# Kernel optimization log

Hardware: AMD Instinct MI355X
Metric: run time of the kernel (lower is better)

## Reference

```python
import jax, jax.numpy as jnp
import numpy as np

N_NODES = 100000
N_EDGES = 1600000
NFEAT, NHID, NCLASS = 512, 256, 128
K_HOPS = 5
ALPHA = 0.1


def setup_inputs() -> dict:
    key = jax.random.key(0)
    ks = jax.random.split(key, 7)
    x = jax.random.normal(ks[0], (N_NODES, NFEAT), dtype=jnp.float32)
    edge_index = jax.random.randint(ks[1], (2, N_EDGES), 0, N_NODES, dtype=jnp.int64)
    edge_weight = jax.random.uniform(ks[2], (N_EDGES,), dtype=jnp.float32)
    # Glorot-ish scaled linear weights
    W1 = jax.random.normal(ks[3], (NFEAT, NHID), dtype=jnp.float32) * (1.0 / np.sqrt(NFEAT))
    b1 = jnp.zeros((NHID,), dtype=jnp.float32)
    W2 = jax.random.normal(ks[4], (NHID, NCLASS), dtype=jnp.float32) * (1.0 / np.sqrt(NHID))
    b2 = jnp.zeros((NCLASS,), dtype=jnp.float32)
    return {"x": x, "edge_index": edge_index, "edge_weight": edge_weight,
            "W1": W1, "b1": b1, "W2": W2, "b2": b2}


def reference(x, edge_index, edge_weight, W1, b1, W2, b2):
    # 2-layer MLP (act after first layer only; dropout p=0)
    h = jnp.maximum(x @ W1 + b1, 0.0)
    h = h @ W2 + b2  # [N, nclass]
    src = edge_index[0]
    dst = edge_index[1]
    x0 = h

    def step(carry, _):
        # gather by source, scale by edge weight, scatter-add at target
        msg = carry[src] * edge_weight[:, None]          # [E, nclass]
        agg = jax.ops.segment_sum(msg, dst, num_segments=N_NODES)
        out = (1.0 - ALPHA) * agg + ALPHA * x0           # restart mix
        return out, None

    xK, _ = jax.lax.scan(step, x0, None, length=K_HOPS)
    return jax.nn.log_softmax(xK, axis=1)
```

## Files before the change

kernel.cpp:

```cpp
#include <hip/hip_runtime.h>
#include <hip/hip_bf16.h>
#include <cstdint>
#include <cstddef>

#define N_NODES 100000
#define NFEAT 512
#define NHID 256
#define NCLASS 128
#define K_HOPS 5
#define ALPHA 0.1f

typedef __attribute__((ext_vector_type(8))) short short8v;
typedef __attribute__((ext_vector_type(4))) float f32x4;

__device__ __forceinline__ unsigned short f2bf(float f) {
    unsigned u = __builtin_bit_cast(unsigned, f);
    u += 0x7FFFu + ((u >> 16) & 1u);
    return (unsigned short)(u >> 16);
}
__device__ __forceinline__ float bflo(unsigned u) {
    return __builtin_bit_cast(float, u << 16);
}
__device__ __forceinline__ float bfhi(unsigned u) {
    return __builtin_bit_cast(float, u & 0xFFFF0000u);
}
__device__ __forceinline__ unsigned cvtpk2(float a, float b) {
    unsigned r;
    asm("v_cvt_pk_bf16_f32 %0, %1, %2" : "=v"(r) : "v"(a), "v"(b));
    return r;
}
__device__ __forceinline__ void gload_lds16(const void* g, void* l) {
    __builtin_amdgcn_global_load_lds((const __attribute__((address_space(1))) void*)g,
                                     (__attribute__((address_space(3))) void*)l, 16, 0, 0);
}


__global__ void count_kernel(const int* __restrict__ dst, int* __restrict__ counts, int E) {
    int i = blockIdx.x * blockDim.x + threadIdx.x;
    if (i < E) atomicAdd(&counts[dst[i]], 1);
}

__global__ __launch_bounds__(256) void scan_p1(const int* __restrict__ counts,
                                               int* __restrict__ partial, int n) {
    __shared__ int ws[4];
    int b = blockIdx.x, t = threadIdx.x;
    int base = b * 1024 + t * 4;
    int s = 0;
#pragma unroll
    for (int j = 0; j < 4; ++j) {
        int idx = base + j;
        if (idx < n) s += counts[idx];
    }
#pragma unroll
    for (int off = 32; off; off >>= 1) s += __shfl_xor(s, off, 64);
    if ((t & 63) == 0) ws[t >> 6] = s;
    __syncthreads();
    if (t == 0) partial[b] = ws[0] + ws[1] + ws[2] + ws[3];
}

__global__ __launch_bounds__(128) void scan_p2(int* __restrict__ partial, int nb) {
    __shared__ int s[128];
    int t = threadIdx.x;
    int v = (t < nb) ? partial[t] : 0;
    s[t] = v;
    __syncthreads();
    for (int off = 1; off < 128; off <<= 1) {
        int u = (t >= off) ? s[t - off] : 0;
        __syncthreads();
        s[t] += u;
        __syncthreads();
    }
    if (t < nb) partial[t] = (t == 0) ? 0 : s[t - 1];
}

__global__ __launch_bounds__(256) void scan_p3(const int* __restrict__ counts,
                                               const int* __restrict__ partial,
                                               int* __restrict__ row_ptr,
                                               int* __restrict__ fill, int n) {
    __shared__ int ts[256];
    int b = blockIdx.x, t = threadIdx.x;
    int base = b * 1024 + t * 4;
    int c[4];
#pragma unroll
    for (int j = 0; j < 4; ++j) {
        int idx = base + j;
        c[j] = (idx < n) ? counts[idx] : 0;
    }
    int s = c[0] + c[1] + c[2] + c[3];
    ts[t] = s;
    __syncthreads();
    for (int off = 1; off < 256; off <<= 1) {
        int v = (t >= off) ? ts[t - off] : 0;
        __syncthreads();
        ts[t] += v;
        __syncthreads();
    }
    int pre = partial[b] + ((t == 0) ? 0 : ts[t - 1]);
#pragma unroll
    for (int j = 0; j < 4; ++j) {
        int idx = base + j;
        if (idx < n) {
            row_ptr[idx] = pre;
            fill[idx] = pre;
            if (idx == n - 1) row_ptr[n] = pre + c[j];
            pre += c[j];
        }
    }
}

__global__ void scatter_kernel(const int* __restrict__ src, const int* __restrict__ dst,
                               const float* __restrict__ w, int* __restrict__ fill,
                               int2* __restrict__ epk, int E) {
    int i = blockIdx.x * blockDim.x + threadIdx.x;
    if (i < E) {
        int d = dst[i];
        int pos = atomicAdd(&fill[d], 1);
        int2 m; m.x = src[i]; m.y = __builtin_bit_cast(int, w[i]);
        epk[pos] = m;
    }
}

__global__ void wtrans_kernel(const float* __restrict__ W, unsigned short* __restrict__ Wt,
                              int K, int N) {
    int idx = blockIdx.x * blockDim.x + threadIdx.x;
    if (idx >= N * K) return;
    int n = idx / K, k = idx - n * K;
    Wt[idx] = f2bf(W[(size_t)k * N + n]);
}

__global__ __launch_bounds__(512) void gemm1_pipe(const float* __restrict__ X,
                                                  const unsigned short* __restrict__ W1t,
                                                  const float* __restrict__ b1,
                                                  unsigned short* __restrict__ Hb, int M) {
    __shared__ char smem[131072];
    char* const Ab0 = smem;
    char* const Bb0 = smem + 65536;

    const int tid = threadIdx.x;
    const int lane = tid & 63;
    const int wv = tid >> 6;
    const int wr = wv >> 2, wc = wv & 3;
    const int brow = blockIdx.x * 128;

    const char* asrc[2];
    int adst[2];
#pragma unroll
    for (int c = 0; c < 2; ++c) {
        int ar = brow + wv * 16 + (lane & 15); if (ar > M - 1) ar = M - 1;
        int k = (lane >> 4) * 8 + c * 4;
        asrc[c] = (const char*)&X[(size_t)ar * NFEAT + k];
        adst[c] = (wv + c * 8) * 1024;
    }
    const char* bsrc[2];
    int bdst[2];
#pragma unroll
    for (int c = 0; c < 2; ++c) {
        int ci = wv + c * 8;
        int col = ci * 16 + (lane & 15);
        bsrc[c] = (const char*)&W1t[(size_t)col * NFEAT + (lane >> 4) * 8];
        bdst[c] = ci * 1024;
    }

    f32x4 acc[4][4];
#pragma unroll
    for (int m = 0; m < 4; ++m)
#pragma unroll
        for (int n = 0; n < 4; ++n) acc[m][n] = f32x4{0.f, 0.f, 0.f, 0.f};

    auto stage = [&](int buf, int step) {
#pragma unroll
        for (int c = 0; c < 2; ++c)
            gload_lds16(asrc[c] + (size_t)step * 128, Ab0 + buf * 16384 + adst[c]);
#pragma unroll
        for (int c = 0; c < 2; ++c)
            gload_lds16(bsrc[c] + (size_t)step * 64, Bb0 + buf * 16384 + bdst[c]);
    };

    constexpr int NSTEP = NFEAT / 32;
    stage(0, 0);
    stage(1, 1);

    for (int s = 0; s < NSTEP; ++s) {
        if (s + 2 < NSTEP) {
            stage((s + 2) & 3, s + 2);
            asm volatile("s_waitcnt vmcnt(8)" ::: "memory");
        } else if (s + 1 < NSTEP) {
            asm volatile("s_waitcnt vmcnt(4)" ::: "memory");
        } else {
            asm volatile("s_waitcnt vmcnt(0)" ::: "memory");
        }
        __builtin_amdgcn_s_barrier();
        asm volatile("" ::: "memory");

        const char* Abuf = Ab0 + (s & 3) * 16384;
        const char* Bbuf = Bb0 + (s & 3) * 16384;
        short8v a[4], b[4];
#pragma unroll
        for (int m = 0; m < 4; ++m) {
            int g = ((wr * 4 + m) * 64 + lane) * 16;
            f32x4 lo = *(const f32x4*)(Abuf + g);
            f32x4 hi = *(const f32x4*)(Abuf + 8192 + g);
            uint4 u;
            u.x = cvtpk2(lo[0], lo[1]); u.y = cvtpk2(lo[2], lo[3]);
            u.z = cvtpk2(hi[0], hi[1]); u.w = cvtpk2(hi[2], hi[3]);
            a[m] = __builtin_bit_cast(short8v, u);
        }
#pragma unroll
        for (int n = 0; n < 4; ++n)
            b[n] = *(const short8v*)(Bbuf + ((wc * 4 + n) * 64 + lane) * 16);
#pragma unroll
        for (int m = 0; m < 4; ++m)
#pragma unroll
            for (int n = 0; n < 4; ++n)
                acc[m][n] = __builtin_amdgcn_mfma_f32_16x16x32_bf16(a[m], b[n], acc[m][n], 0, 0, 0);

        __builtin_amdgcn_s_barrier();
        asm volatile("" ::: "memory");
    }

#pragma unroll
    for (int n = 0; n < 4; ++n) {
        int colg = wc * 64 + n * 16 + (lane & 15);
        float bv = b1[colg];
#pragma unroll
        for (int m = 0; m < 4; ++m) {
#pragma unroll
            for (int r = 0; r < 4; ++r) {
                int rowg = brow + wr * 64 + m * 16 + (lane >> 4) * 4 + r;
                if (rowg < M) {
                    float v = fmaxf(acc[m][n][r] + bv, 0.f);
                    Hb[(size_t)rowg * NHID + colg] = f2bf(v);
                }
            }
        }
    }
}

__global__ __launch_bounds__(256) void gemm2_pipe(const unsigned short* __restrict__ Hb,
                                                  const unsigned short* __restrict__ W2t,
                                                  const float* __restrict__ b2,
                                                  unsigned short* __restrict__ C0, int M) {
    __shared__ char smem[65536];
    char* const Ab0 = smem;
    char* const Bb0 = smem + 32768;

    const int tid = threadIdx.x;
    const int lane = tid & 63;
    const int wv = tid >> 6;
    const int wr = wv >> 1, wc = wv & 1;
    const int brow = blockIdx.x * 128;

    const char* asrc[2];
    const char* bsrc[2];
    int adst[2], bdst[2];
#pragma unroll
    for (int c = 0; c < 2; ++c) {
        int ci = wv + c * 4;
        int ar = brow + ci * 16 + (lane & 15); if (ar > M - 1) ar = M - 1;
        asrc[c] = (const char*)&Hb[(size_t)ar * NHID + (lane >> 4) * 8];
        adst[c] = ci * 1024;
        int col = ci * 16 + (lane & 15);
        bsrc[c] = (const char*)&W2t[(size_t)col * NHID + (lane >> 4) * 8];
        bdst[c] = ci * 1024;
    }

    f32x4 acc[4][4];
#pragma unroll
    for (int m = 0; m < 4; ++m)
#pragma unroll
        for (int n = 0; n < 4; ++n) acc[m][n] = f32x4{0.f, 0.f, 0.f, 0.f};

    auto stage = [&](int buf, int step) {
#pragma unroll
        for (int c = 0; c < 2; ++c)
            gload_lds16(asrc[c] + (size_t)step * 64, Ab0 + buf * 8192 + adst[c]);
#pragma unroll
        for (int c = 0; c < 2; ++c)
            gload_lds16(bsrc[c] + (size_t)step * 64, Bb0 + buf * 8192 + bdst[c]);
    };

    constexpr int NSTEP = NHID / 32;
    stage(0, 0);
    stage(1, 1);

    for (int s = 0; s < NSTEP; ++s) {
        if (s + 2 < NSTEP) {
            stage((s + 2) & 3, s + 2);
            asm volatile("s_waitcnt vmcnt(8)" ::: "memory");
        } else if (s + 1 < NSTEP) {
            asm volatile("s_waitcnt vmcnt(4)" ::: "memory");
        } else {
            asm volatile("s_waitcnt vmcnt(0)" ::: "memory");
        }
        __builtin_amdgcn_s_barrier();
        asm volatile("" ::: "memory");

        const char* Abuf = Ab0 + (s & 3) * 8192;
        const char* Bbuf = Bb0 + (s & 3) * 8192;
        short8v a[4], b[4];
#pragma unroll
        for (int m = 0; m < 4; ++m)
            a[m] = *(const short8v*)(Abuf + ((wr * 4 + m) * 64 + lane) * 16);
#pragma unroll
        for (int n = 0; n < 4; ++n)
            b[n] = *(const short8v*)(Bbuf + ((wc * 4 + n) * 64 + lane) * 16);
#pragma unroll
        for (int m = 0; m < 4; ++m)
#pragma unroll
            for (int n = 0; n < 4; ++n)
                acc[m][n] = __builtin_amdgcn_mfma_f32_16x16x32_bf16(a[m], b[n], acc[m][n], 0, 0, 0);

        __builtin_amdgcn_s_barrier();
        asm volatile("" ::: "memory");
    }

#pragma unroll
    for (int n = 0; n < 4; ++n) {
        int colg = wc * 64 + n * 16 + (lane & 15);
        float bv = b2[colg];
#pragma unroll
        for (int m = 0; m < 4; ++m) {
#pragma unroll
            for (int r = 0; r < 4; ++r) {
                int rowg = brow + wr * 64 + m * 16 + (lane >> 4) * 4 + r;
                if (rowg < M)
                    C0[(size_t)rowg * NCLASS + colg] = f2bf(acc[m][n][r] + bv);
            }
        }
    }
}

template<int FINAL>
__global__ __launch_bounds__(256) void hop_kernel(const unsigned short* __restrict__ carry,
                                                  const unsigned short* __restrict__ c0,
                                                  const int* __restrict__ rp,
                                                  const int2* __restrict__ epk,
                                                  unsigned short* __restrict__ outb,
                                                  float* __restrict__ outf, int nnodes) {
    int node = blockIdx.x * 4 + (threadIdx.x >> 6);
    if (node >= nnodes) return;
    int lane = threadIdx.x & 63;
    int e0 = rp[node], e1 = rp[node + 1];

    float a0x = 0.f, a0y = 0.f, a1x = 0.f, a1y = 0.f;
    float a2x = 0.f, a2y = 0.f, a3x = 0.f, a3y = 0.f;

    for (int eb = e0; eb < e1; eb += 64) {
        int nb = e1 - eb; if (nb > 64) nb = 64;
        int cs = 0, wvi = 0;
        if (lane < nb) {
            int2 m = epk[eb + lane];
            cs = m.x; wvi = m.y;
        }
        int j = 0;
        for (; j + 7 < nb; j += 8) {
            int s0 = __builtin_amdgcn_readlane(cs, j);
            int s1 = __builtin_amdgcn_readlane(cs, j + 1);
            int s2 = __builtin_amdgcn_readlane(cs, j + 2);
            int s3 = __builtin_amdgcn_readlane(cs, j + 3);
            int s4 = __builtin_amdgcn_readlane(cs, j + 4);
            int s5 = __builtin_amdgcn_readlane(cs, j + 5);
            int s6 = __builtin_amdgcn_readlane(cs, j + 6);
            int s7 = __builtin_amdgcn_readlane(cs, j + 7);
            float w0 = __builtin_bit_cast(float, __builtin_amdgcn_readlane(wvi, j));
            float w1 = __builtin_bit_cast(float, __builtin_amdgcn_readlane(wvi, j + 1));
            float w2 = __builtin_bit_cast(float, __builtin_amdgcn_readlane(wvi, j + 2));
            float w3 = __builtin_bit_cast(float, __builtin_amdgcn_readlane(wvi, j + 3));
            float w4 = __builtin_bit_cast(float, __builtin_amdgcn_readlane(wvi, j + 4));
            float w5 = __builtin_bit_cast(float, __builtin_amdgcn_readlane(wvi, j + 5));
            float w6 = __builtin_bit_cast(float, __builtin_amdgcn_readlane(wvi, j + 6));
            float w7 = __builtin_bit_cast(float, __builtin_amdgcn_readlane(wvi, j + 7));
            unsigned u0 = ((const unsigned*)(carry + ((size_t)s0 << 7)))[lane];
            unsigned u1 = ((const unsigned*)(carry + ((size_t)s1 << 7)))[lane];
            unsigned u2 = ((const unsigned*)(carry + ((size_t)s2 << 7)))[lane];
            unsigned u3 = ((const unsigned*)(carry + ((size_t)s3 << 7)))[lane];
            unsigned u4 = ((const unsigned*)(carry + ((size_t)s4 << 7)))[lane];
            unsigned u5 = ((const unsigned*)(carry + ((size_t)s5 << 7)))[lane];
            unsigned u6 = ((const unsigned*)(carry + ((size_t)s6 << 7)))[lane];
            unsigned u7 = ((const unsigned*)(carry + ((size_t)s7 << 7)))[lane];
            a0x = fmaf(w0, bflo(u0), a0x); a0y = fmaf(w0, bfhi(u0), a0y);
            a1x = fmaf(w1, bflo(u1), a1x); a1y = fmaf(w1, bfhi(u1), a1y);
            a2x = fmaf(w2, bflo(u2), a2x); a2y = fmaf(w2, bfhi(u2), a2y);
            a3x = fmaf(w3, bflo(u3), a3x); a3y = fmaf(w3, bfhi(u3), a3y);
            a0x = fmaf(w4, bflo(u4), a0x); a0y = fmaf(w4, bfhi(u4), a0y);
            a1x = fmaf(w5, bflo(u5), a1x); a1y = fmaf(w5, bfhi(u5), a1y);
            a2x = fmaf(w6, bflo(u6), a2x); a2y = fmaf(w6, bfhi(u6), a2y);
            a3x = fmaf(w7, bflo(u7), a3x); a3y = fmaf(w7, bfhi(u7), a3y);
        }
        for (; j + 3 < nb; j += 4) {
            int s0 = __builtin_amdgcn_readlane(cs, j);
            int s1 = __builtin_amdgcn_readlane(cs, j + 1);
            int s2 = __builtin_amdgcn_readlane(cs, j + 2);
            int s3 = __builtin_amdgcn_readlane(cs, j + 3);
            float w0 = __builtin_bit_cast(float, __builtin_amdgcn_readlane(wvi, j));
            float w1 = __builtin_bit_cast(float, __builtin_amdgcn_readlane(wvi, j + 1));
            float w2 = __builtin_bit_cast(float, __builtin_amdgcn_readlane(wvi, j + 2));
            float w3 = __builtin_bit_cast(float, __builtin_amdgcn_readlane(wvi, j + 3));
            unsigned u0 = ((const unsigned*)(carry + ((size_t)s0 << 7)))[lane];
            unsigned u1 = ((const unsigned*)(carry + ((size_t)s1 << 7)))[lane];
            unsigned u2 = ((const unsigned*)(carry + ((size_t)s2 << 7)))[lane];
            unsigned u3 = ((const unsigned*)(carry + ((size_t)s3 << 7)))[lane];
            a0x = fmaf(w0, bflo(u0), a0x); a0y = fmaf(w0, bfhi(u0), a0y);
            a1x = fmaf(w1, bflo(u1), a1x); a1y = fmaf(w1, bfhi(u1), a1y);
            a2x = fmaf(w2, bflo(u2), a2x); a2y = fmaf(w2, bfhi(u2), a2y);
            a3x = fmaf(w3, bflo(u3), a3x); a3y = fmaf(w3, bfhi(u3), a3y);
        }
        for (; j < nb; ++j) {
            int s0 = __builtin_amdgcn_readlane(cs, j);
            float w0 = __builtin_bit_cast(float, __builtin_amdgcn_readlane(wvi, j));
            unsigned u0 = ((const unsigned*)(carry + ((size_t)s0 << 7)))[lane];
            a0x = fmaf(w0, bflo(u0), a0x); a0y = fmaf(w0, bfhi(u0), a0y);
        }
    }

    unsigned ux = ((const unsigned*)(c0 + ((size_t)node << 7)))[lane];
    float vx = (1.f - ALPHA) * (a0x + a1x + a2x + a3x) + ALPHA * bflo(ux);
    float vy = (1.f - ALPHA) * (a0y + a1y + a2y + a3y) + ALPHA * bfhi(ux);

    if (FINAL) {
        float mx = fmaxf(vx, vy);
#pragma unroll
        for (int off = 32; off; off >>= 1) mx = fmaxf(mx, __shfl_xor(mx, off, 64));
        float se = __expf(vx - mx) + __expf(vy - mx);
#pragma unroll
        for (int off = 32; off; off >>= 1) se += __shfl_xor(se, off, 64);
        float l = mx + __logf(se);
        float2 o; o.x = vx - l; o.y = vy - l;
        ((float2*)(outf + ((size_t)node << 7)))[lane] = o;
    } else {
        unsigned o = (unsigned)f2bf(vx) | ((unsigned)f2bf(vy) << 16);
        ((unsigned*)(outb + ((size_t)node << 7)))[lane] = o;
    }
}


extern "C" void kernel_launch(void* const* d_in, const int* in_sizes, int n_in,
                              void* d_out, int out_size, void* d_ws, size_t ws_size,
                              hipStream_t stream) {
    const float* x   = (const float*)d_in[0];
    const int*   ei  = (const int*)d_in[1];
    const float* ew  = (const float*)d_in[2];
    const float* W1  = (const float*)d_in[3];
    const float* b1  = (const float*)d_in[4];
    const float* W2  = (const float*)d_in[5];
    const float* b2  = (const float*)d_in[6];
    float* outp = (float*)d_out;

    const int E = in_sizes[1] / 2;
    const int Nn = N_NODES;
    const int* srcv = ei;
    const int* dstv = ei + E;
    const size_t NC = (size_t)Nn * NCLASS;

    unsigned short* c0  = (unsigned short*)d_ws;
    unsigned short* A16 = c0 + NC;
    unsigned short* B16 = A16 + NC;
    unsigned short* hb  = A16;
    unsigned short* w1t = B16 + NC;
    unsigned short* w2t = w1t + NHID * NFEAT;
    int* row_ptr = (int*)(w2t + NCLASS * NHID);
    int* fill    = row_ptr + (Nn + 1);
    int* partial = fill + Nn;
    int2* epk    = (int2*)(partial + 128);

    const int NB = (Nn + 1023) / 1024;

    hipMemsetAsync(fill, 0, (size_t)Nn * sizeof(int), stream);
    count_kernel<<<(E + 255) / 256, 256, 0, stream>>>(dstv, fill, E);
    scan_p1<<<NB, 256, 0, stream>>>(fill, partial, Nn);
    scan_p2<<<1, 128, 0, stream>>>(partial, NB);
    scan_p3<<<NB, 256, 0, stream>>>(fill, partial, row_ptr, fill, Nn);
    scatter_kernel<<<(E + 255) / 256, 256, 0, stream>>>(srcv, dstv, ew, fill, epk, E);

    wtrans_kernel<<<(NHID * NFEAT + 255) / 256, 256, 0, stream>>>(W1, w1t, NFEAT, NHID);
    wtrans_kernel<<<(NCLASS * NHID + 255) / 256, 256, 0, stream>>>(W2, w2t, NHID, NCLASS);

    {
        int gm = (Nn + 127) / 128;
        gemm1_pipe<<<gm, 512, 0, stream>>>(x, w1t, b1, hb, Nn);
        gemm2_pipe<<<gm, 256, 0, stream>>>(hb, w2t, b2, c0, Nn);
    }

    int grid = (Nn + 3) / 4;
    const unsigned short* carry = c0;
    unsigned short* dsts[2] = {A16, B16};
    for (int k = 0; k < K_HOPS - 1; ++k) {
        unsigned short* o = dsts[k & 1];
        hop_kernel<0><<<grid, 256, 0, stream>>>(carry, c0, row_ptr, epk, o, nullptr, Nn);
        carry = o;
    }
    hop_kernel<1><<<grid, 256, 0, stream>>>(carry, c0, row_ptr, epk, nullptr, outp, Nn);
}
```

Baseline: 640.4 us.

## Split hop gather into 4 column groups with edge-parallel subwaves

The SpMM hop kernel is restructured so each wave handles one 64-byte column slice (32 features) of a node, with a grid dimension over 4 column groups. The 4 sub-groups of 16 lanes each process different edges in parallel and reduce with cross-lane shuffles. The aim is more memory-level parallelism and more waves for short-degree nodes. The cost is that each node's edge list and row pointers are read 4 times, and 3/4 of the lanes sit idle on the epilogue. Log-softmax moves to a separate kernel, which adds an extra pass over the output.

After: 0.9996 ms. +56.1%, slower.

```diff
diff --git a/kernel.cpp b/kernel.cpp
--- a/kernel.cpp
+++ b/kernel.cpp
@@ -331,106 +331,80 @@
 }
 
 template<int FINAL>
-__global__ __launch_bounds__(256) void hop_kernel(const unsigned short* __restrict__ carry,
-                                                  const unsigned short* __restrict__ c0,
-                                                  const int* __restrict__ rp,
-                                                  const int2* __restrict__ epk,
-                                                  unsigned short* __restrict__ outb,
-                                                  float* __restrict__ outf, int nnodes) {
+__global__ __launch_bounds__(256) void hop_grp(const unsigned short* __restrict__ carry,
+                                               const unsigned short* __restrict__ c0,
+                                               const int* __restrict__ rp,
+                                               const int2* __restrict__ epk,
+                                               unsigned short* __restrict__ outb,
+                                               float* __restrict__ outf, int nnodes) {
+    int node = blockIdx.x * 4 + (threadIdx.x >> 6);
+    if (node >= nnodes) return;
+    const int g = blockIdx.y;
+    const int lane = threadIdx.x & 63;
+    const int sub = lane >> 4;
+    const int c = lane & 15;
+    const int gbase = g * 16 + c;
+    const unsigned* cu = (const unsigned*)carry;
+
+    int e0 = rp[node], e1 = rp[node + 1];
+    float ax = 0.f, ay = 0.f;
+
+    for (int eb = e0; eb < e1; eb += 64) {
+        int nb = e1 - eb; if (nb > 64) nb = 64;
+        int cs = 0, wv = 0;
+        if (lane < nb) {
+            int2 m = epk[eb + lane];
+            cs = m.x; wv = m.y;
+        }
+        for (int j = 0; j < nb; j += 16) {
+            int i0 = j + sub, i1 = i0 + 4, i2 = i0 + 8, i3 = i0 + 12;
+            int s0 = __shfl(cs, i0, 64); float w0 = __builtin_bit_cast(float, __shfl(wv, i0, 64));
+            int s1 = __shfl(cs, i1, 64); float w1 = __builtin_bit_cast(float, __shfl(wv, i1, 64));
+            int s2 = __shfl(cs, i2, 64); float w2 = __builtin_bit_cast(float, __shfl(wv, i2, 64));
+            int s3 = __shfl(cs, i3, 64); float w3 = __builtin_bit_cast(float, __shfl(wv, i3, 64));
+            unsigned u0 = cu[(size_t)s0 * 64 + gbase];
+            unsigned u1 = cu[(size_t)s1 * 64 + gbase];
+            unsigned u2 = cu[(size_t)s2 * 64 + gbase];
+            unsigned u3 = cu[(size_t)s3 * 64 + gbase];
+            ax = fmaf(w0, bflo(u0), ax); ay = fmaf(w0, bfhi(u0), ay);
+            ax = fmaf(w1, bflo(u1), ax); ay = fmaf(w1, bfhi(u1), ay);
+            ax = fmaf(w2, bflo(u2), ax); ay = fmaf(w2, bfhi(u2), ay);
+            ax = fmaf(w3, bflo(u3), ax); ay = fmaf(w3, bfhi(u3), ay);
+        }
+    }
+
+    ax += __shfl_xor(ax, 16, 64); ax += __shfl_xor(ax, 32, 64);
+    ay += __shfl_xor(ay, 16, 64); ay += __shfl_xor(ay, 32, 64);
+
+    if (lane < 16) {
+        unsigned u = ((const unsigned*)c0)[(size_t)node * 64 + gbase];
+        float vx = (1.f - ALPHA) * ax + ALPHA * bflo(u);
+        float vy = (1.f - ALPHA) * ay + ALPHA * bfhi(u);
+        if (FINAL) {
+            float2 o; o.x = vx; o.y = vy;
+            ((float2*)outf)[(size_t)node * 64 + gbase] = o;
+        } else {
+            ((unsigned*)outb)[(size_t)node * 64 + gbase] =
+                (unsigned)f2bf(vx) | ((unsigned)f2bf(vy) << 16);
+        }
+    }
+}
+
+__global__ __launch_bounds__(256) void logsoftmax_kernel(float* __restrict__ buf, int nnodes) {
     int node = blockIdx.x * 4 + (threadIdx.x >> 6);
     if (node >= nnodes) return;
     int lane = threadIdx.x & 63;
-    int e0 = rp[node], e1 = rp[node + 1];
-
-    float a0x = 0.f, a0y = 0.f, a1x = 0.f, a1y = 0.f;
-    float a2x = 0.f, a2y = 0.f, a3x = 0.f, a3y = 0.f;
-
-    for (int eb = e0; eb < e1; eb += 64) {
-        int nb = e1 - eb; if (nb > 64) nb = 64;
-        int cs = 0, wvi = 0;
-        if (lane < nb) {
-            int2 m = epk[eb + lane];
-            cs = m.x; wvi = m.y;
-        }
-        int j = 0;
-        for (; j + 7 < nb; j += 8) {
-            int s0 = __builtin_amdgcn_readlane(cs, j);
-            int s1 = __builtin_amdgcn_readlane(cs, j + 1);
-            int s2 = __builtin_amdgcn_readlane(cs, j + 2);
-            int s3 = __builtin_amdgcn_readlane(cs, j + 3);
-            int s4 = __builtin_amdgcn_readlane(cs, j + 4);
-            int s5 = __builtin_amdgcn_readlane(cs, j + 5);
-            int s6 = __builtin_amdgcn_readlane(cs, j + 6);
-            int s7 = __builtin_amdgcn_readlane(cs, j + 7);
-            float w0 = __builtin_bit_cast(float, __builtin_amdgcn_readlane(wvi, j));
-            float w1 = __builtin_bit_cast(float, __builtin_amdgcn_readlane(wvi, j + 1));
-            float w2 = __builtin_bit_cast(float, __builtin_amdgcn_readlane(wvi, j + 2));
-            float w3 = __builtin_bit_cast(float, __builtin_amdgcn_readlane(wvi, j + 3));
-            float w4 = __builtin_bit_cast(float, __builtin_amdgcn_readlane(wvi, j + 4));
-            float w5 = __builtin_bit_cast(float, __builtin_amdgcn_readlane(wvi, j + 5));
-            float w6 = __builtin_bit_cast(float, __builtin_amdgcn_readlane(wvi, j + 6));
-            float w7 = __builtin_bit_cast(float, __builtin_amdgcn_readlane(wvi, j + 7));
-            unsigned u0 = ((const unsigned*)(carry + ((size_t)s0 << 7)))[lane];
-            unsigned u1 = ((const unsigned*)(carry + ((size_t)s1 << 7)))[lane];
-            unsigned u2 = ((const unsigned*)(carry + ((size_t)s2 << 7)))[lane];
-            unsigned u3 = ((const unsigned*)(carry + ((size_t)s3 << 7)))[lane];
-            unsigned u4 = ((const unsigned*)(carry + ((size_t)s4 << 7)))[lane];
-            unsigned u5 = ((const unsigned*)(carry + ((size_t)s5 << 7)))[lane];
-            unsigned u6 = ((const unsigned*)(carry + ((size_t)s6 << 7)))[lane];
-            unsigned u7 = ((const unsigned*)(carry + ((size_t)s7 << 7)))[lane];
-            a0x = fmaf(w0, bflo(u0), a0x); a0y = fmaf(w0, bfhi(u0), a0y);
-            a1x = fmaf(w1, bflo(u1), a1x); a1y = fmaf(w1, bfhi(u1), a1y);
-            a2x = fmaf(w2, bflo(u2), a2x); a2y = fmaf(w2, bfhi(u2), a2y);
-            a3x = fmaf(w3, bflo(u3), a3x); a3y = fmaf(w3, bfhi(u3), a3y);
-            a0x = fmaf(w4, bflo(u4), a0x); a0y = fmaf(w4, bfhi(u4), a0y);
-            a1x = fmaf(w5, bflo(u5), a1x); a1y = fmaf(w5, bfhi(u5), a1y);
-            a2x = fmaf(w6, bflo(u6), a2x); a2y = fmaf(w6, bfhi(u6), a2y);
-            a3x = fmaf(w7, bflo(u7), a3x); a3y = fmaf(w7, bfhi(u7), a3y);
-        }
-        for (; j + 3 < nb; j += 4) {
-            int s0 = __builtin_amdgcn_readlane(cs, j);
-            int s1 = __builtin_amdgcn_readlane(cs, j + 1);
-            int s2 = __builtin_amdgcn_readlane(cs, j + 2);
-            int s3 = __builtin_amdgcn_readlane(cs, j + 3);
-            float w0 = __builtin_bit_cast(float, __builtin_amdgcn_readlane(wvi, j));
-            float w1 = __builtin_bit_cast(float, __builtin_amdgcn_readlane(wvi, j + 1));
-            float w2 = __builtin_bit_cast(float, __builtin_amdgcn_readlane(wvi, j + 2));
-            float w3 = __builtin_bit_cast(float, __builtin_amdgcn_readlane(wvi, j + 3));
-            unsigned u0 = ((const unsigned*)(carry + ((size_t)s0 << 7)))[lane];
-            unsigned u1 = ((const unsigned*)(carry + ((size_t)s1 << 7)))[lane];
-            unsigned u2 = ((const unsigned*)(carry + ((size_t)s2 << 7)))[lane];
-            unsigned u3 = ((const unsigned*)(carry + ((size_t)s3 << 7)))[lane];
-            a0x = fmaf(w0, bflo(u0), a0x); a0y = fmaf(w0, bfhi(u0), a0y);
-            a1x = fmaf(w1, bflo(u1), a1x); a1y = fmaf(w1, bfhi(u1), a1y);
-            a2x = fmaf(w2, bflo(u2), a2x); a2y = fmaf(w2, bfhi(u2), a2y);
-            a3x = fmaf(w3, bflo(u3), a3x); a3y = fmaf(w3, bfhi(u3), a3y);
-        }
-        for (; j < nb; ++j) {
-            int s0 = __builtin_amdgcn_readlane(cs, j);
-            float w0 = __builtin_bit_cast(float, __builtin_amdgcn_readlane(wvi, j));
-            unsigned u0 = ((const unsigned*)(carry + ((size_t)s0 << 7)))[lane];
-            a0x = fmaf(w0, bflo(u0), a0x); a0y = fmaf(w0, bfhi(u0), a0y);
-        }
-    }
-
-    unsigned ux = ((const unsigned*)(c0 + ((size_t)node << 7)))[lane];
-    float vx = (1.f - ALPHA) * (a0x + a1x + a2x + a3x) + ALPHA * bflo(ux);
-    float vy = (1.f - ALPHA) * (a0y + a1y + a2y + a3y) + ALPHA * bfhi(ux);
-
-    if (FINAL) {
-        float mx = fmaxf(vx, vy);
-#pragma unroll
-        for (int off = 32; off; off >>= 1) mx = fmaxf(mx, __shfl_xor(mx, off, 64));
-        float se = __expf(vx - mx) + __expf(vy - mx);
-#pragma unroll
-        for (int off = 32; off; off >>= 1) se += __shfl_xor(se, off, 64);
-        float l = mx + __logf(se);
-        float2 o; o.x = vx - l; o.y = vy - l;
-        ((float2*)(outf + ((size_t)node << 7)))[lane] = o;
-    } else {
-        unsigned o = (unsigned)f2bf(vx) | ((unsigned)f2bf(vy) << 16);
-        ((unsigned*)(outb + ((size_t)node << 7)))[lane] = o;
-    }
+    float2* p = (float2*)(buf + ((size_t)node << 7)) + lane;
+    float2 v = *p;
+    float m = fmaxf(v.x, v.y);
+#pragma unroll
+    for (int off = 32; off; off >>= 1) m = fmaxf(m, __shfl_xor(m, off, 64));
+    float s = __expf(v.x - m) + __expf(v.y - m);
+#pragma unroll
+    for (int off = 32; off; off >>= 1) s += __shfl_xor(s, off, 64);
+    float l = m + __logf(s);
+    float2 o; o.x = v.x - l; o.y = v.y - l;
+    *p = o;
 }
 
 
@@ -481,13 +455,15 @@
         gemm2_pipe<<<gm, 256, 0, stream>>>(hb, w2t, b2, c0, Nn);
     }
 
-    int grid = (Nn + 3) / 4;
+    dim3 gh((Nn + 3) / 4, 4);
     const unsigned short* carry = c0;
     unsigned short* dsts[2] = {A16, B16};
     for (int k = 0; k < K_HOPS - 1; ++k) {
         unsigned short* o = dsts[k & 1];
-        hop_kernel<0><<<grid, 256, 0, stream>>>(carry, c0, row_ptr, epk, o, nullptr, Nn);
+        hop_grp<0><<<gh, 256, 0, stream>>>(carry, c0, row_ptr, epk, o, nullptr, Nn);
         carry = o;
     }
-    hop_kernel<1><<<grid, 256, 0, stream>>>(carry, c0, row_ptr, epk, nullptr, outp, Nn);
-}
+    hop_grp<1><<<gh, 256, 0, stream>>>(carry, c0, row_ptr, epk, nullptr, outp, Nn);
+
+    logsoftmax_kernel<<<(Nn + 3) / 4, 256, 0, stream>>>(outp, Nn);
+}
```

## Replace multi-buffered GEMM pipelines with single-buffer, smaller-tile GEMM kernels

Applied to the files above, without the earlier changes.

Both MLP GEMM kernels drop the 4-stage async LDS pipeline in favour of a simple load, wait, sync, compute loop with a single LDS buffer. GEMM1 also splits the 256 output columns over two blocks, using 256-thread blocks with 128x128 tiles instead of 512-thread blocks covering all 256 columns. This cuts LDS use per block (128KB to 24KB, 64KB to 16KB) so more blocks can be resident, relying on occupancy rather than software prefetch to hide latency. The cost is exposed load latency inside each block and GEMM1 reading the fp32 X tiles twice.

New measurement: 691.0 us. 1.08x slower.

```diff
diff --git a/kernel.cpp b/kernel.cpp
--- a/kernel.cpp
+++ b/kernel.cpp
@@ -128,35 +128,37 @@
     Wt[idx] = f2bf(W[(size_t)k * N + n]);
 }
 
-__global__ __launch_bounds__(512) void gemm1_pipe(const float* __restrict__ X,
-                                                  const unsigned short* __restrict__ W1t,
-                                                  const float* __restrict__ b1,
-                                                  unsigned short* __restrict__ Hb, int M) {
-    __shared__ char smem[131072];
-    char* const Ab0 = smem;
-    char* const Bb0 = smem + 65536;
+__global__ __launch_bounds__(256) void gemm1_m97(const float* __restrict__ X,
+                                                 const unsigned short* __restrict__ W1t,
+                                                 const float* __restrict__ b1,
+                                                 unsigned short* __restrict__ Hb, int M) {
+    __shared__ char smem[24576];
+    char* const Abuf = smem;
+    char* const Bbuf = smem + 16384;
 
     const int tid = threadIdx.x;
     const int lane = tid & 63;
     const int wv = tid >> 6;
-    const int wr = wv >> 2, wc = wv & 3;
-    const int brow = blockIdx.x * 128;
-
-    const char* asrc[2];
-    int adst[2];
-#pragma unroll
-    for (int c = 0; c < 2; ++c) {
-        int ar = brow + wv * 16 + (lane & 15); if (ar > M - 1) ar = M - 1;
-        int k = (lane >> 4) * 8 + c * 4;
-        asrc[c] = (const char*)&X[(size_t)ar * NFEAT + k];
-        adst[c] = (wv + c * 8) * 1024;
+    const int wr = wv >> 1, wc = wv & 1;
+    const int bcol = blockIdx.x * 128;
+    const int brow = blockIdx.y * 128;
+
+    const char* asrc[4];
+    int adst[4];
+#pragma unroll
+    for (int c = 0; c < 4; ++c) {
+        int ci = wv + c * 4;
+        int sub = ci & 7, plane = ci >> 3;
+        int ar = brow + sub * 16 + (lane & 15); if (ar > M - 1) ar = M - 1;
+        asrc[c] = (const char*)&X[(size_t)ar * NFEAT + (lane >> 4) * 8 + plane * 4];
+        adst[c] = ci * 1024;
     }
     const char* bsrc[2];
     int bdst[2];
 #pragma unroll
     for (int c = 0; c < 2; ++c) {
-        int ci = wv + c * 8;
-        int col = ci * 16 + (lane & 15);
+        int ci = wv + c * 4;
+        int col = bcol + ci * 16 + (lane & 15);
         bsrc[c] = (const char*)&W1t[(size_t)col * NFEAT + (lane >> 4) * 8];
         bdst[c] = ci * 1024;
     }
@@ -167,33 +169,16 @@
 #pragma unroll
         for (int n = 0; n < 4; ++n) acc[m][n] = f32x4{0.f, 0.f, 0.f, 0.f};
 
-    auto stage = [&](int buf, int step) {
+    for (int s = 0; s < NFEAT / 32; ++s) {
+#pragma unroll
+        for (int c = 0; c < 4; ++c)
+            gload_lds16(asrc[c] + (size_t)s * 128, Abuf + adst[c]);
 #pragma unroll
         for (int c = 0; c < 2; ++c)
-            gload_lds16(asrc[c] + (size_t)step * 128, Ab0 + buf * 16384 + adst[c]);
-#pragma unroll
-        for (int c = 0; c < 2; ++c)
-            gload_lds16(bsrc[c] + (size_t)step * 64, Bb0 + buf * 16384 + bdst[c]);
-    };
-
-    constexpr int NSTEP = NFEAT / 32;
-    stage(0, 0);
-    stage(1, 1);
-
-    for (int s = 0; s < NSTEP; ++s) {
-        if (s + 2 < NSTEP) {
-            stage((s + 2) & 3, s + 2);
-            asm volatile("s_waitcnt vmcnt(8)" ::: "memory");
-        } else if (s + 1 < NSTEP) {
-            asm volatile("s_waitcnt vmcnt(4)" ::: "memory");
-        } else {
-            asm volatile("s_waitcnt vmcnt(0)" ::: "memory");
-        }
-        __builtin_amdgcn_s_barrier();
-        asm volatile("" ::: "memory");
-
-        const char* Abuf = Ab0 + (s & 3) * 16384;
-        const char* Bbuf = Bb0 + (s & 3) * 16384;
+            gload_lds16(bsrc[c] + (size_t)s * 64, Bbuf + bdst[c]);
+        asm volatile("s_waitcnt vmcnt(0)" ::: "memory");
+        __syncthreads();
+
         short8v a[4], b[4];
 #pragma unroll
         for (int m = 0; m < 4; ++m) {
@@ -213,14 +198,12 @@
 #pragma unroll
             for (int n = 0; n < 4; ++n)
                 acc[m][n] = __builtin_amdgcn_mfma_f32_16x16x32_bf16(a[m], b[n], acc[m][n], 0, 0, 0);
-
-        __builtin_amdgcn_s_barrier();
-        asm volatile("" ::: "memory");
+        __syncthreads();
     }
 
 #pragma unroll
     for (int n = 0; n < 4; ++n) {
-        int colg = wc * 64 + n * 16 + (lane & 15);
+        int colg = bcol + wc * 64 + n * 16 + (lane & 15);
         float bv = b1[colg];
 #pragma unroll
         for (int m = 0; m < 4; ++m) {
@@ -236,13 +219,13 @@
     }
 }
 
-__global__ __launch_bounds__(256) void gemm2_pipe(const unsigned short* __restrict__ Hb,
-                                                  const unsigned short* __restrict__ W2t,
-                                                  const float* __restrict__ b2,
-                                                  unsigned short* __restrict__ C0, int M) {
-    __shared__ char smem[65536];
-    char* const Ab0 = smem;
-    char* const Bb0 = smem + 32768;
+__global__ __launch_bounds__(256) void gemm2_m97(const unsigned short* __restrict__ Hb,
+                                                 const unsigned short* __restrict__ W2t,
+                                                 const float* __restrict__ b2,
+                                                 unsigned short* __restrict__ C0, int M) {
+    __shared__ char smem[16384];
+    char* const Abuf = smem;
+    char* const Bbuf = smem + 8192;
 
     const int tid = threadIdx.x;
     const int lane = tid & 63;
@@ -252,16 +235,15 @@
 
     const char* asrc[2];
     const char* bsrc[2];
-    int adst[2], bdst[2];
+    int cdst[2];
 #pragma unroll
     for (int c = 0; c < 2; ++c) {
         int ci = wv + c * 4;
         int ar = brow + ci * 16 + (lane & 15); if (ar > M - 1) ar = M - 1;
         asrc[c] = (const char*)&Hb[(size_t)ar * NHID + (lane >> 4) * 8];
-        adst[c] = ci * 1024;
         int col = ci * 16 + (lane & 15);
         bsrc[c] = (const char*)&W2t[(size_t)col * NHID + (lane >> 4) * 8];
-        bdst[c] = ci * 1024;
+        cdst[c] = ci * 1024;
     }
 
     f32x4 acc[4][4];
@@ -270,33 +252,15 @@
 #pragma unroll
         for (int n = 0; n < 4; ++n) acc[m][n] = f32x4{0.f, 0.f, 0.f, 0.f};
 
-    auto stage = [&](int buf, int step) {
-#pragma unroll
-        for (int c = 0; c < 2; ++c)
-            gload_lds16(asrc[c] + (size_t)step * 64, Ab0 + buf * 8192 + adst[c]);
-#pragma unroll
-        for (int c = 0; c < 2; ++c)
-            gload_lds16(bsrc[c] + (size_t)step * 64, Bb0 + buf * 8192 + bdst[c]);
-    };
-
-    constexpr int NSTEP = NHID / 32;
-    stage(0, 0);
-    stage(1, 1);
-
-    for (int s = 0; s < NSTEP; ++s) {
-        if (s + 2 < NSTEP) {
-            stage((s + 2) & 3, s + 2);
-            asm volatile("s_waitcnt vmcnt(8)" ::: "memory");
-        } else if (s + 1 < NSTEP) {
-            asm volatile("s_waitcnt vmcnt(4)" ::: "memory");
-        } else {
-            asm volatile("s_waitcnt vmcnt(0)" ::: "memory");
-        }
-        __builtin_amdgcn_s_barrier();
-        asm volatile("" ::: "memory");
-
-        const char* Abuf = Ab0 + (s & 3) * 8192;
-        const char* Bbuf = Bb0 + (s & 3) * 8192;
+    for (int s = 0; s < NHID / 32; ++s) {
+#pragma unroll
+        for (int c = 0; c < 2; ++c) {
+            gload_lds16(asrc[c] + (size_t)s * 64, Abuf + cdst[c]);
+            gload_lds16(bsrc[c] + (size_t)s * 64, Bbuf + cdst[c]);
+        }
+        asm volatile("s_waitcnt vmcnt(0)" ::: "memory");
+        __syncthreads();
+
         short8v a[4], b[4];
 #pragma unroll
         for (int m = 0; m < 4; ++m)
@@ -309,9 +273,7 @@
 #pragma unroll
             for (int n = 0; n < 4; ++n)
                 acc[m][n] = __builtin_amdgcn_mfma_f32_16x16x32_bf16(a[m], b[n], acc[m][n], 0, 0, 0);
-
-        __builtin_amdgcn_s_barrier();
-        asm volatile("" ::: "memory");
+        __syncthreads();
     }
 
 #pragma unroll
@@ -476,9 +438,9 @@
     wtrans_kernel<<<(NCLASS * NHID + 255) / 256, 256, 0, stream>>>(W2, w2t, NHID, NCLASS);
 
     {
-        int gm = (Nn + 127) / 128;
-        gemm1_pipe<<<gm, 512, 0, stream>>>(x, w1t, b1, hb, Nn);
-        gemm2_pipe<<<gm, 256, 0, stream>>>(hb, w2t, b2, c0, Nn);
+        dim3 g1(2, (Nn + 127) / 128);
+        gemm1_m97<<<g1, 256, 0, stream>>>(x, w1t, b1, hb, Nn);
+        gemm2_m97<<<(Nn + 127) / 128, 256, 0, stream>>>(hb, w2t, b2, c0, Nn);
     }
 
     int grid = (Nn + 3) / 4;
```
